# Kernel tuning notes

Measured on AMD Instinct MI355X. Metric: run time of the kernel, lower is better.

## Reference

```python
import jax, jax.numpy as jnp
import numpy as np

N_QUBITS = 4
N_LAYERS = 6
BATCH = 1 << 20


def _apply_batched_1q(state, U, q):
    # state: [B, 2,2,2,2]; U: [B, 2, 2] per-sample gate on qubit q
    ax = q + 1
    s = jnp.moveaxis(state, ax, -1)
    s = jnp.einsum('bij,b...j->b...i', U, s)
    return jnp.moveaxis(s, -1, ax)


def _apply_shared_1q(state, U, q):
    # U: [2, 2] shared across the batch
    ax = q + 1
    s = jnp.moveaxis(state, ax, -1)
    s = jnp.einsum('ij,...j->...i', U, s)
    return jnp.moveaxis(s, -1, ax)


def _cnot(state, c, t):
    # flip target axis on the control=1 slice
    ca, ta = c + 1, t + 1
    s0 = jax.lax.index_in_dim(state, 0, ca, keepdims=True)
    s1 = jax.lax.index_in_dim(state, 1, ca, keepdims=True)
    return jnp.concatenate([s0, jnp.flip(s1, axis=ta)], axis=ca)


def _circuit(x, weights):
    n = N_QUBITS
    B = x.shape[0]
    # |0...0> state, batched: [B, 2,2,2,2]
    state = jnp.zeros((B,) + (2,) * n, dtype=jnp.complex64)
    state = state.at[(slice(None),) + (0,) * n].set(1.0)
    # Data-encoding RY(x_q) per sample on each wire
    half = x / 2
    c, s = jnp.cos(half), jnp.sin(half)  # [B, n]
    for q in range(n):
        row0 = jnp.stack([c[:, q], -s[:, q]], axis=-1)
        row1 = jnp.stack([s[:, q], c[:, q]], axis=-1)
        U = jnp.stack([row0, row1], axis=-2).astype(jnp.complex64)  # [B,2,2]
        state = _apply_batched_1q(state, U, q)
    # BasicEntanglerLayers: per layer, RX(w) on each wire then CNOT ring
    for l in range(weights.shape[0]):
        for q in range(n):
            t = weights[l, q] / 2
            ct = (jnp.cos(t) + 0j).astype(jnp.complex64)
            st = (-1j * jnp.sin(t)).astype(jnp.complex64)
            U = jnp.stack([jnp.stack([ct, st]), jnp.stack([st, ct])])  # [2,2]
            state = _apply_shared_1q(state, U, q)
        for q in range(n):
            state = _cnot(state, q, (q + 1) % n)
    # <Z_q> from marginal probabilities
    probs = jnp.real(state * jnp.conj(state))  # [B,2,2,2,2] float32
    z = jnp.array([1.0, -1.0], dtype=jnp.float32)
    outs = []
    for q in range(n):
        reduce_axes = tuple(a for a in range(1, n + 1) if a != q + 1)
        outs.append(jnp.tensordot(probs.sum(axis=reduce_axes), z, axes=([1], [0])))
    return jnp.stack(outs, axis=-1)  # [B, n_qubits]


def setup_inputs():
    key = jax.random.key(0)
    k1, k2 = jax.random.split(key)
    x = jax.random.normal(k1, (BATCH, N_QUBITS), dtype=jnp.float32)
    weights = jax.random.normal(k2, (N_LAYERS, N_QUBITS), dtype=jnp.float32) * 0.01
    return {"x": x, "weights": weights}


def reference(x, weights):
    return _circuit(x, weights)
```

## Files before the change

kernel.cpp:

```cpp
#include <hip/hip_runtime.h>
#include <math.h>

#define N_QUBITS 4
#define N_LAYERS 6
#define NW (N_LAYERS * N_QUBITS)

__global__ __launch_bounds__(256) void qlayer_kernel(
    const float* __restrict__ x,
    const float* __restrict__ weights,
    float* __restrict__ out,
    int B)
{
    __shared__ float wc[NW];
    __shared__ float ws[NW];
    const int tid = threadIdx.x;
    if (tid < NW) {
        float t = weights[tid] * 0.5f;
        wc[tid] = __cosf(t);
        ws[tid] = __sinf(t);
    }
    __syncthreads();

    const int b = blockIdx.x * blockDim.x + tid;
    if (b >= B) return;

    const float4 xv = reinterpret_cast<const float4*>(x)[b];
    float cx[4], sx[4];
    {
        float h0 = xv.x * 0.5f, h1 = xv.y * 0.5f, h2 = xv.z * 0.5f, h3 = xv.w * 0.5f;
        cx[0] = __cosf(h0); sx[0] = __sinf(h0);
        cx[1] = __cosf(h1); sx[1] = __sinf(h1);
        cx[2] = __cosf(h2); sx[2] = __sinf(h2);
        cx[3] = __cosf(h3); sx[3] = __sinf(h3);
    }

    float re[16], im[16];
#pragma unroll
    for (int idx = 0; idx < 16; ++idx) {
        float a = ((idx & 8) ? sx[0] : cx[0]) * ((idx & 4) ? sx[1] : cx[1]);
        a *= ((idx & 2) ? sx[2] : cx[2]) * ((idx & 1) ? sx[3] : cx[3]);
        re[idx] = a;
        im[idx] = 0.0f;
    }

#pragma unroll
    for (int l = 0; l < N_LAYERS; ++l) {
#pragma unroll
        for (int q = 0; q < N_QUBITS; ++q) {
            const float ct = wc[l * 4 + q];
            const float sn = ws[l * 4 + q];
            const int mask = 8 >> q;
#pragma unroll
            for (int idx = 0; idx < 16; ++idx) {
                if (idx & mask) continue;
                const int j = idx | mask;
                const float r0 = re[idx], u0 = im[idx];
                const float r1 = re[j],   u1 = im[j];
                re[idx] = ct * r0 + sn * u1;
                im[idx] = ct * u0 - sn * r1;
                re[j]   = ct * r1 + sn * u0;
                im[j]   = ct * u1 - sn * r0;
            }
        }
#pragma unroll
        for (int q = 0; q < N_QUBITS; ++q) {
            const int cmask = 8 >> q;
            const int tmask = 8 >> ((q + 1) & 3);
#pragma unroll
            for (int idx = 0; idx < 16; ++idx) {
                if ((idx & cmask) && !(idx & tmask)) {
                    const int j = idx | tmask;
                    float tr = re[idx]; re[idx] = re[j]; re[j] = tr;
                    float ti = im[idx]; im[idx] = im[j]; im[j] = ti;
                }
            }
        }
    }

    float z0 = 0.f, z1 = 0.f, z2 = 0.f, z3 = 0.f;
#pragma unroll
    for (int idx = 0; idx < 16; ++idx) {
        const float p = re[idx] * re[idx] + im[idx] * im[idx];
        z0 += (idx & 8) ? -p : p;
        z1 += (idx & 4) ? -p : p;
        z2 += (idx & 2) ? -p : p;
        z3 += (idx & 1) ? -p : p;
    }
    reinterpret_cast<float4*>(out)[b] = make_float4(z0, z1, z2, z3);
}

extern "C" void kernel_launch(void* const* d_in, const int* in_sizes, int n_in,
                              void* d_out, int out_size, void* d_ws, size_t ws_size,
                              hipStream_t stream) {
    const float* x = (const float*)d_in[0];
    const float* weights = (const float*)d_in[1];
    float* out = (float*)d_out;
    const int B = in_sizes[0] / 4;

    const int block = 256;
    const int grid = (B + block - 1) / block;
    qlayer_kernel<<<grid, block, 0, stream>>>(x, weights, out, B);
}
```

Measured before the change: 99.45 us.

## Precompute circuit observable as trig-polynomial coefficient table, evaluate per sample

A single-block prep kernel builds the fixed entangling unitary from the weights, forms the Heisenberg-picture Z observables, and expands them into 81 coefficients per qubit over the basis {1, cos x, sin x} for each input wire. The main kernel then computes each output as a nested fused-multiply-add contraction over that table, using full-angle cos and sin of x. This replaces the per-sample 16-amplitude complex state simulation with far less arithmetic. It adds a second launch and relies on a workspace buffer plus uniform table loads.

```diff
diff --git a/kernel.cpp b/kernel.cpp
--- a/kernel.cpp
+++ b/kernel.cpp
@@ -5,88 +5,122 @@
 #define N_LAYERS 6
 #define NW (N_LAYERS * N_QUBITS)
 
-__global__ __launch_bounds__(256) void qlayer_kernel(
-    const float* __restrict__ x,
-    const float* __restrict__ weights,
-    float* __restrict__ out,
-    int B)
+__global__ __launch_bounds__(256) void qprep_kernel(
+    const float* __restrict__ weights, float* __restrict__ Ctab)
 {
-    __shared__ float wc[NW];
-    __shared__ float ws[NW];
+    __shared__ float Wr[16][16];
+    __shared__ float Wi[16][16];
+    __shared__ float S[4][16][16];
+    __shared__ float wc[NW], ws[NW];
     const int tid = threadIdx.x;
     if (tid < NW) {
         float t = weights[tid] * 0.5f;
-        wc[tid] = __cosf(t);
-        ws[tid] = __sinf(t);
+        wc[tid] = cosf(t);
+        ws[tid] = sinf(t);
     }
     __syncthreads();
 
-    const int b = blockIdx.x * blockDim.x + tid;
-    if (b >= B) return;
-
-    const float4 xv = reinterpret_cast<const float4*>(x)[b];
-    float cx[4], sx[4];
-    {
-        float h0 = xv.x * 0.5f, h1 = xv.y * 0.5f, h2 = xv.z * 0.5f, h3 = xv.w * 0.5f;
-        cx[0] = __cosf(h0); sx[0] = __sinf(h0);
-        cx[1] = __cosf(h1); sx[1] = __sinf(h1);
-        cx[2] = __cosf(h2); sx[2] = __sinf(h2);
-        cx[3] = __cosf(h3); sx[3] = __sinf(h3);
-    }
-
-    float re[16], im[16];
-#pragma unroll
-    for (int idx = 0; idx < 16; ++idx) {
-        float a = ((idx & 8) ? sx[0] : cx[0]) * ((idx & 4) ? sx[1] : cx[1]);
-        a *= ((idx & 2) ? sx[2] : cx[2]) * ((idx & 1) ? sx[3] : cx[3]);
-        re[idx] = a;
-        im[idx] = 0.0f;
-    }
-
-#pragma unroll
-    for (int l = 0; l < N_LAYERS; ++l) {
-#pragma unroll
-        for (int q = 0; q < N_QUBITS; ++q) {
-            const float ct = wc[l * 4 + q];
-            const float sn = ws[l * 4 + q];
-            const int mask = 8 >> q;
-#pragma unroll
-            for (int idx = 0; idx < 16; ++idx) {
-                if (idx & mask) continue;
-                const int j = idx | mask;
-                const float r0 = re[idx], u0 = im[idx];
-                const float r1 = re[j],   u1 = im[j];
-                re[idx] = ct * r0 + sn * u1;
-                im[idx] = ct * u0 - sn * r1;
-                re[j]   = ct * r1 + sn * u0;
-                im[j]   = ct * u1 - sn * r0;
+    if (tid < 16) {
+        float re[16], im[16];
+        for (int k = 0; k < 16; ++k) { re[k] = (k == tid) ? 1.f : 0.f; im[k] = 0.f; }
+        for (int l = 0; l < N_LAYERS; ++l) {
+            for (int q = 0; q < 4; ++q) {
+                const float ct = wc[l * 4 + q], sn = ws[l * 4 + q];
+                const int mask = 8 >> q;
+                for (int idx = 0; idx < 16; ++idx) {
+                    if (idx & mask) continue;
+                    const int j = idx | mask;
+                    float r0 = re[idx], u0 = im[idx], r1 = re[j], u1 = im[j];
+                    re[idx] = ct * r0 + sn * u1; im[idx] = ct * u0 - sn * r1;
+                    re[j]   = ct * r1 + sn * u0; im[j]   = ct * u1 - sn * r0;
+                }
             }
-        }
-#pragma unroll
-        for (int q = 0; q < N_QUBITS; ++q) {
-            const int cmask = 8 >> q;
-            const int tmask = 8 >> ((q + 1) & 3);
-#pragma unroll
-            for (int idx = 0; idx < 16; ++idx) {
-                if ((idx & cmask) && !(idx & tmask)) {
-                    const int j = idx | tmask;
-                    float tr = re[idx]; re[idx] = re[j]; re[j] = tr;
-                    float ti = im[idx]; im[idx] = im[j]; im[j] = ti;
+            for (int q = 0; q < 4; ++q) {
+                const int cm = 8 >> q, tm = 8 >> ((q + 1) & 3);
+                for (int idx = 0; idx < 16; ++idx) {
+                    if ((idx & cm) && !(idx & tm)) {
+                        const int j = idx | tm;
+                        float t0 = re[idx]; re[idx] = re[j]; re[j] = t0;
+                        float t1 = im[idx]; im[idx] = im[j]; im[j] = t1;
+                    }
                 }
             }
         }
+        for (int k = 0; k < 16; ++k) { Wr[k][tid] = re[k]; Wi[k][tid] = im[k]; }
     }
+    __syncthreads();
 
-    float z0 = 0.f, z1 = 0.f, z2 = 0.f, z3 = 0.f;
+    {
+        const int i = tid >> 4, j = tid & 15;
+        float acc[4] = {0.f, 0.f, 0.f, 0.f};
+        for (int k = 0; k < 16; ++k) {
+            const float prod = Wr[k][i] * Wr[k][j] + Wi[k][i] * Wi[k][j];
+            for (int q = 0; q < 4; ++q)
+                acc[q] += (k & (8 >> q)) ? -prod : prod;
+        }
+        for (int q = 0; q < 4; ++q) S[q][i][j] = acc[q];
+    }
+    __syncthreads();
+
+    if (tid < 81) {
+        const int t1 = tid / 27, t2 = (tid / 9) % 3, t3 = (tid / 3) % 3, t4 = tid % 3;
+        const int tp[4] = {t1, t2, t3, t4};
+        int zm = 0, xm = 0;
+        for (int p = 0; p < 4; ++p) {
+            if (tp[p] == 1)      zm |= (8 >> p);
+            else if (tp[p] == 2) xm |= (8 >> p);
+        }
+        for (int q = 0; q < 4; ++q) {
+            float acc = 0.f;
+            for (int i = 0; i < 16; ++i) {
+                const float v = S[q][i][i ^ xm];
+                acc += (__popc(i & zm) & 1) ? -v : v;
+            }
+            Ctab[q * 81 + tid] = acc * 0.0625f;
+        }
+    }
+}
+
+__global__ __launch_bounds__(256) void qeval_kernel(
+    const float* __restrict__ x, const float* __restrict__ Ctab,
+    float* __restrict__ out, int B)
+{
+    const int b = blockIdx.x * blockDim.x + threadIdx.x;
+    if (b >= B) return;
+    const float4 xv = reinterpret_cast<const float4*>(x)[b];
+
+    float v0[3], v1[3], v2[3], v3[3];
+    v0[0] = 1.f; v0[1] = __cosf(xv.x); v0[2] = __sinf(xv.x);
+    v1[0] = 1.f; v1[1] = __cosf(xv.y); v1[2] = __sinf(xv.y);
+    v2[0] = 1.f; v2[1] = __cosf(xv.z); v2[2] = __sinf(xv.z);
+    v3[0] = 1.f; v3[1] = __cosf(xv.w); v3[2] = __sinf(xv.w);
+
+    float o[4];
 #pragma unroll
-    for (int idx = 0; idx < 16; ++idx) {
-        const float p = re[idx] * re[idx] + im[idx] * im[idx];
-        z0 += (idx & 8) ? -p : p;
-        z1 += (idx & 4) ? -p : p;
-        z2 += (idx & 2) ? -p : p;
-        z3 += (idx & 1) ? -p : p;
+    for (int q = 0; q < 4; ++q) {
+        const float* __restrict__ Cq = Ctab + q * 81;
+        float s1 = 0.f;
+#pragma unroll
+        for (int t1 = 0; t1 < 3; ++t1) {
+            float s2 = 0.f;
+#pragma unroll
+            for (int t2 = 0; t2 < 3; ++t2) {
+                float s3 = 0.f;
+#pragma unroll
+                for (int t3 = 0; t3 < 3; ++t3) {
+                    const int base = ((t1 * 3 + t2) * 3 + t3) * 3;
+                    float e = Cq[base];
+                    e = fmaf(Cq[base + 1], v3[1], e);
+                    e = fmaf(Cq[base + 2], v3[2], e);
+                    s3 = (t3 == 0) ? (s3 + e) : fmaf(e, v2[t3], s3);
+                }
+                s2 = (t2 == 0) ? (s2 + s3) : fmaf(s3, v1[t2], s2);
+            }
+            s1 = (t1 == 0) ? (s1 + s2) : fmaf(s2, v0[t1], s1);
+        }
+        o[q] = s1;
     }
-    reinterpret_cast<float4*>(out)[b] = make_float4(z0, z1, z2, z3);
+    reinterpret_cast<float4*>(out)[b] = make_float4(o[0], o[1], o[2], o[3]);
 }
 
 extern "C" void kernel_launch(void* const* d_in, const int* in_sizes, int n_in,
@@ -95,9 +129,12 @@
     const float* x = (const float*)d_in[0];
     const float* weights = (const float*)d_in[1];
     float* out = (float*)d_out;
+    float* Ctab = (float*)d_ws;
     const int B = in_sizes[0] / 4;
+
+    qprep_kernel<<<1, 256, 0, stream>>>(weights, Ctab);
 
     const int block = 256;
     const int grid = (B + block - 1) / block;
-    qlayer_kernel<<<grid, block, 0, stream>>>(x, weights, out, B);
+    qeval_kernel<<<grid, block, 0, stream>>>(x, Ctab, out, B);
 }
```

After: 83.04 us. 1.2x faster.
